# Optimization experiments

Hardware: AMD Instinct MI355X
Metric: run time of the kernel (lower is better)

## Reference

```python
import jax, jax.numpy as jnp
import numpy as np

B, H, W, C = 32, 56, 56, 192
WS, SS, NH = 7, 3, 6  # window, shift, heads
N = WS * WS
HIDDEN = int(C * 4.0)
TABLE = (2 * WS - 1) * (2 * WS - 1)  # 169
EPS = 1e-5

# Relative position index, faithful to the source (meshgrid default 'xy',
# and the source multiplies BOTH coord channels by (2*ws-1), so indices can
# exceed the table size; gather uses clip like jnp.take's jit behavior).
_coords = np.stack(np.meshgrid(np.arange(WS), np.arange(WS))).reshape(2, -1)
_rel = (_coords[:, :, None] - _coords[:, None, :]).transpose(1, 2, 0)
_rel = (_rel + WS - 1) * (2 * WS - 1)
REL_IDX = jnp.asarray(_rel.sum(-1))  # [N, N]

# Shift attention mask (static), labels regions then marks cross-region pairs.
_m = np.zeros((H, W))
_cnt = 0
for hs in [slice(0, -WS), slice(-WS, -SS), slice(-SS, None)]:
    for ws_ in [slice(0, -WS), slice(-WS, -SS), slice(-SS, None)]:
        _m[hs, ws_] = _cnt
        _cnt += 1
_mw = _m.reshape(H // WS, WS, W // WS, WS).transpose(0, 2, 1, 3).reshape(-1, N)
ATTN_MASK = jnp.asarray((_mw[:, None, :] != _mw[:, :, None]).astype(np.float32))  # [nW, N, N]
NW = ATTN_MASK.shape[0]


def layer_norm(x, g, b):
    mu = jnp.mean(x, axis=-1, keepdims=True)
    xc = x - mu
    var = jnp.mean(xc * xc, axis=-1, keepdims=True)
    return xc * jax.lax.rsqrt(var + EPS) * g + b


def window_partition(x):  # [B,H,W,C] -> [B*nW, N, C]
    x = x.reshape(B, H // WS, WS, W // WS, WS, C).transpose(0, 1, 3, 2, 4, 5)
    return x.reshape(-1, N, C)


def window_reverse(w):  # [B*nW, N, C] -> [B,H,W,C]
    x = w.reshape(B, H // WS, W // WS, WS, WS, C).transpose(0, 1, 3, 2, 4, 5)
    return x.reshape(B, H, W, C)


def setup_inputs() -> dict:
    key = jax.random.key(0)
    ks = jax.random.split(key, 16)
    s = lambda fan_in: 1.0 / np.sqrt(fan_in)
    return {
        "x": jax.random.normal(ks[0], (B, H * W, C), jnp.float32),
        "norm1_g": jnp.ones((C,), jnp.float32),
        "norm1_b": jnp.zeros((C,), jnp.float32),
        "qkv_w": jax.random.normal(ks[1], (C, 3 * C), jnp.float32) * s(C),
        "qkv_b": jnp.zeros((3 * C,), jnp.float32),
        "rel_table": jax.random.normal(ks[2], (TABLE, NH), jnp.float32) * 0.02,
        "proj_w": jax.random.normal(ks[3], (C, C), jnp.float32) * s(C),
        "proj_b": jnp.zeros((C,), jnp.float32),
        "norm2_g": jnp.ones((C,), jnp.float32),
        "norm2_b": jnp.zeros((C,), jnp.float32),
        "fc1_w": jax.random.normal(ks[4], (C, HIDDEN), jnp.float32) * s(C),
        "fc1_b": jnp.zeros((HIDDEN,), jnp.float32),
        "fc2_w": jax.random.normal(ks[5], (HIDDEN, C), jnp.float32) * s(HIDDEN),
        "fc2_b": jnp.zeros((C,), jnp.float32),
    }


def reference(x, norm1_g, norm1_b, qkv_w, qkv_b, rel_table, proj_w, proj_b,
              norm2_g, norm2_b, fc1_w, fc1_b, fc2_w, fc2_b):
    shortcut = x
    h = layer_norm(x, norm1_g, norm1_b).reshape(B, H, W, C)
    # cyclic shift
    h = jnp.roll(h, shift=(-SS, -SS), axis=(1, 2))
    xw = window_partition(h)  # [B*nW, N, C]

    # window attention
    qkv = xw @ qkv_w + qkv_b  # [B*nW, N, 3C]
    q, k, v = jnp.split(qkv, 3, axis=-1)
    hd = C // NH
    q = q.reshape(-1, N, NH, hd).transpose(0, 2, 1, 3) * (hd ** -0.5)
    k = k.reshape(-1, N, NH, hd).transpose(0, 2, 1, 3)
    v = v.reshape(-1, N, NH, hd).transpose(0, 2, 1, 3)
    attn = jnp.einsum("whnd,whmd->whnm", q, k)  # [B*nW, NH, N, N]
    bias = jnp.take(rel_table, REL_IDX, axis=0, mode="clip")  # [N,N,NH]
    attn = attn + bias.transpose(2, 0, 1)[None]
    attn = attn.reshape(B, NW, NH, N, N) + ATTN_MASK[None, :, None] * -100.0
    attn = jax.nn.softmax(attn.reshape(-1, NH, N, N), axis=-1)
    o = jnp.einsum("whnm,whmd->whnd", attn, v)
    o = o.transpose(0, 2, 1, 3).reshape(-1, N, C)
    o = o @ proj_w + proj_b

    h = window_reverse(o)
    h = jnp.roll(h, shift=(SS, SS), axis=(1, 2)).reshape(B, H * W, C)
    x = shortcut + h
    # MLP
    m = layer_norm(x, norm2_g, norm2_b)
    m = jax.nn.gelu(m @ fc1_w + fc1_b, approximate=False) @ fc2_w + fc2_b
    return x + m
```

## Files before the change

kernel.cpp:

```cpp
#include <hip/hip_runtime.h>
#include <hip/hip_bf16.h>


using f32x4  = __attribute__((ext_vector_type(4))) float;
using short8 = __attribute__((ext_vector_type(8))) short;
typedef unsigned short ushort_t;

__device__ __forceinline__ ushort_t f2bf(float f) {
    __hip_bfloat16 h = __float2bfloat16(f);
    return __builtin_bit_cast(ushort_t, h);
}
__device__ __forceinline__ f32x4 mfma16(short8 a, short8 b, f32x4 c) {
    return __builtin_amdgcn_mfma_f32_16x16x32_bf16(a, b, c, 0, 0, 0);
}
__device__ __forceinline__ float fast_gelu(float h) {
    float hh = h * h;
    float p  = __builtin_fmaf(hh, 0.044715f, 1.0f);
    float z  = h * (-1.5957691216057308f);
    float em = __expf(p * z);
    return h * __builtin_amdgcn_rcpf(1.0f + em);
}

#define CC 192

#define OFF_QKVT   0
#define OFF_PROJT  221184
#define OFF_FC1T   294912
#define OFF_FC2T   589824
#define OFF_BIAS   884736
#define OFF_MASK   942592
#define OFF_BMT    1557504
#define OFF_QG     7848960
#define OFF_KG     46384128
#define OFF_VG     84919296
#define WS_NEED    123454464
#define PREP_SMALL 610438
#define PREP_BIG   2183302

__global__ void prep_kernel(const float* __restrict__ qkv_w, const float* __restrict__ proj_w,
                            const float* __restrict__ fc1_w, const float* __restrict__ fc2_w,
                            const float* __restrict__ rel_table,
                            ushort_t* __restrict__ qkvT, ushort_t* __restrict__ projT,
                            ushort_t* __restrict__ fc1T, ushort_t* __restrict__ fc2T,
                            float* __restrict__ biasT, float* __restrict__ maskT,
                            float* __restrict__ bmT, int full) {
    int idx = blockIdx.x * 256 + threadIdx.x;
    if (idx < 110592) { int n = idx / 192, k = idx % 192; qkvT[idx] = f2bf(qkv_w[k * 576 + n]); return; }
    idx -= 110592;
    if (idx < 36864) { int n = idx / 192, k = idx % 192; projT[idx] = f2bf(proj_w[k * 192 + n]); return; }
    idx -= 36864;
    if (idx < 147456) { int n = idx / 192, k = idx % 192; fc1T[idx] = f2bf(fc1_w[k * 768 + n]); return; }
    idx -= 147456;
    if (idx < 147456) { int n = idx / 768, k = idx % 768; fc2T[idx] = f2bf(fc2_w[k * 192 + n]); return; }
    idx -= 147456;
    if (idx < 14406) {
        int h = idx / 2401; int rest = idx % 2401; int a = rest / 49, b = rest % 49;
        int d = 13 * ((a % 7) - (b % 7) + (a / 7) - (b / 7) + 12);
        if (d > 168) d = 168;
        biasT[idx] = rel_table[d * 6 + h];
        return;
    }
    idx -= 14406;
    if (idx < 153664) {
        int w = idx / 2401; int rest = idx % 2401; int a = rest / 49, b = rest % 49;
        int wy = w / 8, wx = w % 8;
        int ya = wy * 7 + a / 7, xa = wx * 7 + a % 7;
        int yb = wy * 7 + b / 7, xb = wx * 7 + b % 7;
        int lya = ya < 49 ? 0 : (ya < 53 ? 1 : 2);
        int lxa = xa < 49 ? 0 : (xa < 53 ? 1 : 2);
        int lyb = yb < 49 ? 0 : (yb < 53 ? 1 : 2);
        int lxb = xb < 49 ? 0 : (xb < 53 ? 1 : 2);
        maskT[idx] = ((lya * 3 + lxa) != (lyb * 3 + lxb)) ? -100.0f : 0.0f;
        return;
    }
    idx -= 153664;
    if (full && idx < 1572864) {
        int wi = idx / 24576; int r2 = idx % 24576;
        int h = r2 / 4096; int r3 = r2 % 4096;
        int col = r3 / 64, row = r3 % 64;
        float v = -1e30f;
        if (row < 49 && col < 49) {
            int d = 13 * ((row % 7) - (col % 7) + (row / 7) - (col / 7) + 12);
            if (d > 168) d = 168;
            float bias = rel_table[d * 6 + h];
            int wy = wi / 8, wx = wi % 8;
            int ya = wy * 7 + row / 7, xa = wx * 7 + row % 7;
            int yb = wy * 7 + col / 7, xb = wx * 7 + col % 7;
            int lya = ya < 49 ? 0 : (ya < 53 ? 1 : 2);
            int lxa = xa < 49 ? 0 : (xa < 53 ? 1 : 2);
            int lyb = yb < 49 ? 0 : (yb < 53 ? 1 : 2);
            int lxb = xb < 49 ? 0 : (xb < 53 ? 1 : 2);
            float mask = ((lya * 3 + lxa) != (lyb * 3 + lxb)) ? -100.0f : 0.0f;
            v = bias + mask;
        }
        bmT[idx] = v;
        return;
    }
}

__global__ __launch_bounds__(256, 3) void lnqkv_kernel(
    const float* __restrict__ x, const float* __restrict__ n1g, const float* __restrict__ n1b,
    const ushort_t* __restrict__ qkvT, const float* __restrict__ qkv_b,
    ushort_t* __restrict__ qg, ushort_t* __restrict__ kg, ushort_t* __restrict__ vg) {
    __shared__ ushort_t xln [64 * 200];
    __shared__ ushort_t qkvs[64 * 200];
    const int tid = threadIdx.x;
    const int wave = tid >> 6, lane = tid & 63;
    const int ln16 = lane & 15, sub = lane >> 4;
    const int t0 = blockIdx.x * 64;
    const f32x4 zero4 = {0.f, 0.f, 0.f, 0.f};

    {
        float g0 = n1g[lane], g1 = n1g[lane + 64], g2 = n1g[lane + 128];
        float bb0 = n1b[lane], bb1 = n1b[lane + 64], bb2 = n1b[lane + 128];
        for (int rb = 0; rb < 4; ++rb) {
            int row0 = wave * 16 + rb * 4;
            float v0[4], v1[4], v2[4], s[4], q[4];
            #pragma unroll
            for (int j = 0; j < 4; ++j) {
                const float* xr = x + (size_t)(t0 + row0 + j) * CC;
                v0[j] = xr[lane]; v1[j] = xr[lane + 64]; v2[j] = xr[lane + 128];
            }
            #pragma unroll
            for (int j = 0; j < 4; ++j) {
                s[j] = v0[j] + v1[j] + v2[j];
                q[j] = v0[j] * v0[j] + v1[j] * v1[j] + v2[j] * v2[j];
            }
            #pragma unroll
            for (int m = 32; m; m >>= 1) {
                #pragma unroll
                for (int j = 0; j < 4; ++j) { s[j] += __shfl_xor(s[j], m); q[j] += __shfl_xor(q[j], m); }
            }
            #pragma unroll
            for (int j = 0; j < 4; ++j) {
                float mu = s[j] * (1.0f / 192.0f);
                float var = q[j] * (1.0f / 192.0f) - mu * mu;
                float rs = rsqrtf(var + 1e-5f);
                int row = row0 + j;
                xln[row * 200 + lane]       = f2bf((v0[j] - mu) * rs * g0 + bb0);
                xln[row * 200 + lane + 64]  = f2bf((v1[j] - mu) * rs * g1 + bb1);
                xln[row * 200 + lane + 128] = f2bf((v2[j] - mu) * rs * g2 + bb2);
            }
        }
    }
    __syncthreads();

    ushort_t* dsts[3] = {qg, kg, vg};
    for (int v = 0; v < 3; ++v) {
        f32x4 acc[4][3];
        #pragma unroll
        for (int m = 0; m < 4; ++m)
            #pragma unroll
            for (int n = 0; n < 3; ++n) acc[m][n] = zero4;
        for (int kk = 0; kk < 6; ++kk) {
            short8 a[4];
            #pragma unroll
            for (int m = 0; m < 4; ++m)
                a[m] = *(const short8*)(xln + (m * 16 + ln16) * 200 + kk * 32 + 8 * sub);
            #pragma unroll
            for (int n = 0; n < 3; ++n) {
                short8 b = *(const short8*)(qkvT + (size_t)(v * 192 + (wave * 3 + n) * 16 + ln16) * 192 + kk * 32 + 8 * sub);
                #pragma unroll
                for (int m = 0; m < 4; ++m) acc[m][n] = mfma16(a[m], b, acc[m][n]);
            }
        }
        #pragma unroll
        for (int n = 0; n < 3; ++n) {
            int col = (wave * 3 + n) * 16 + ln16;
            float bv = qkv_b[v * 192 + col];
            #pragma unroll
            for (int m = 0; m < 4; ++m)
                #pragma unroll
                for (int r = 0; r < 4; ++r) {
                    int row = m * 16 + 4 * sub + r;
                    float val = acc[m][n][r] + bv;
                    if (v == 0) val *= 0.17677669529663689f;
                    qkvs[row * 200 + col] = f2bf(val);
                }
        }
        __syncthreads();
        ushort_t* dst = dsts[v];
        for (int i = tid; i < 1536; i += 256) {
            int row = i / 24, c = i % 24;
            short8 vv = *(const short8*)(qkvs + row * 200 + c * 8);
            *(short8*)(dst + (size_t)(t0 + row) * 192 + c * 8) = vv;
        }
        __syncthreads();
    }
}

__global__ __launch_bounds__(256, 3) void attnmlp_kernel(
    const float* __restrict__ x, const float* __restrict__ proj_b,
    const ushort_t* __restrict__ qg, const ushort_t* __restrict__ kg,
    const ushort_t* __restrict__ vg, const ushort_t* __restrict__ projT,
    const float* __restrict__ bmT,
    const float* __restrict__ n2g, const float* __restrict__ n2b,
    const float* __restrict__ fc1_b, const float* __restrict__ fc2_b,
    const ushort_t* __restrict__ fc1T, const ushort_t* __restrict__ fc2T,
    float* __restrict__ out) {
    __shared__ __align__(16) char smem[51200];
    ushort_t* vt   = (ushort_t*)smem;
    ushort_t* PO   = (ushort_t*)(smem + 27648);
    ushort_t* aln  = (ushort_t*)smem;
    ushort_t* hidc = (ushort_t*)(smem + 25600);
    float*    fout = (float*)smem;

    const int tid = threadIdx.x;
    const int wave = tid >> 6, lane = tid & 63;
    const int ln16 = lane & 15, sub = lane >> 4;
    const int win = blockIdx.x;
    const int b = win >> 6, wi = win & 63;
    const int wy = wi >> 3, wx = wi & 7;
    const f32x4 zero4 = {0.f, 0.f, 0.f, 0.f};

    size_t tokA;
    {
        int j = wave * 16 + ln16; if (j > 48) j = 48;
        int y  = wy * 7 + j / 7 + 3; if (y >= 56) y -= 56;
        int xx = wx * 7 + j % 7 + 3; if (xx >= 56) xx -= 56;
        tokA = (size_t)(b * 3136 + y * 56 + xx);
    }
    size_t tokB[4];
    #pragma unroll
    for (int n = 0; n < 4; ++n) {
        int j = n * 16 + ln16; if (j > 48) j = 48;
        int y  = wy * 7 + j / 7 + 3; if (y >= 56) y -= 56;
        int xx = wx * 7 + j % 7 + 3; if (xx >= 56) xx -= 56;
        tokB[n] = (size_t)(b * 3136 + y * 56 + xx);
    }
    const float* bmw = bmT + (size_t)wi * 24576 + (size_t)(wave * 16 + 4 * sub);

    short8 qf = *(const short8*)(qg + tokA * 192 + 8 * sub);
    short8 kf[4];
    f32x4  bv[4];
    #pragma unroll
    for (int n = 0; n < 4; ++n) {
        kf[n] = *(const short8*)(kg + tokB[n] * 192 + 8 * sub);
        bv[n] = *(const f32x4*)(bmw + (n * 16 + ln16) * 64);
    }

    {
        int j = tid & 63;
        int jj = j < 49 ? j : 48;
        int y  = wy * 7 + jj / 7 + 3; if (y >= 56) y -= 56;
        int xx = wx * 7 + jj % 7 + 3; if (xx >= 56) xx -= 56;
        size_t tokV = (size_t)(b * 3136 + y * 56 + xx);
        const bool valid = j < 49;
        #pragma unroll
        for (int pass = 0; pass < 6; ++pass) {
            int c8 = pass * 32 + (tid >> 6) * 8;
            if (valid) {
                short8 vv = *(const short8*)(vg + tokV * 192 + c8);
                #pragma unroll
                for (int q = 0; q < 8; ++q) vt[(c8 + q) * 72 + j] = ((ushort_t*)&vv)[q];
            } else {
                #pragma unroll
                for (int q = 0; q < 8; ++q) vt[(c8 + q) * 72 + j] = 0;
            }
        }
    }

    f32x4 accP[12];
    #pragma unroll
    for (int n = 0; n < 12; ++n) accP[n] = zero4;
    ushort_t* Pw = PO + wave * (16 * 72);
    __syncthreads();

    #pragma unroll
    for (int h = 0; h < 6; ++h) {
        f32x4 s4[4];
        #pragma unroll
        for (int n = 0; n < 4; ++n) s4[n] = mfma16(qf, kf[n], zero4);
        short8 qn; short8 kn[4]; f32x4 bn[4];
        if (h < 5) {
            qn = *(const short8*)(qg + tokA * 192 + (h + 1) * 32 + 8 * sub);
            #pragma unroll
            for (int n = 0; n < 4; ++n) {
                kn[n] = *(const short8*)(kg + tokB[n] * 192 + (h + 1) * 32 + 8 * sub);
                bn[n] = *(const f32x4*)(bmw + (h + 1) * 4096 + (n * 16 + ln16) * 64);
            }
        }
        #pragma unroll
        for (int n = 0; n < 4; ++n)
            #pragma unroll
            for (int r = 0; r < 4; ++r) s4[n][r] += bv[n][r];
        #pragma unroll
        for (int r = 0; r < 4; ++r) {
            float mx = fmaxf(fmaxf(s4[0][r], s4[1][r]), fmaxf(s4[2][r], s4[3][r]));
            mx = fmaxf(mx, __shfl_xor(mx, 1, 16));
            mx = fmaxf(mx, __shfl_xor(mx, 2, 16));
            mx = fmaxf(mx, __shfl_xor(mx, 4, 16));
            mx = fmaxf(mx, __shfl_xor(mx, 8, 16));
            float e0 = __expf(s4[0][r] - mx), e1 = __expf(s4[1][r] - mx);
            float e2 = __expf(s4[2][r] - mx), e3 = __expf(s4[3][r] - mx);
            float sm = e0 + e1 + e2 + e3;
            sm += __shfl_xor(sm, 1, 16);
            sm += __shfl_xor(sm, 2, 16);
            sm += __shfl_xor(sm, 4, 16);
            sm += __shfl_xor(sm, 8, 16);
            float inv = 1.0f / sm;
            int rl = 4 * sub + r;
            Pw[rl * 72 +      ln16] = f2bf(e0 * inv);
            Pw[rl * 72 + 16 + ln16] = f2bf(e1 * inv);
            Pw[rl * 72 + 32 + ln16] = f2bf(e2 * inv);
            Pw[rl * 72 + 48 + ln16] = f2bf(e3 * inv);
        }
        short8 ap0 = *(const short8*)(Pw + ln16 * 72 + 8 * sub);
        short8 ap1 = *(const short8*)(Pw + ln16 * 72 + 32 + 8 * sub);
        f32x4 o2[2]; o2[0] = zero4; o2[1] = zero4;
        #pragma unroll
        for (int n2 = 0; n2 < 2; ++n2) {
            short8 bv0 = *(const short8*)(vt + (h * 32 + n2 * 16 + ln16) * 72 + 8 * sub);
            short8 bv1 = *(const short8*)(vt + (h * 32 + n2 * 16 + ln16) * 72 + 32 + 8 * sub);
            o2[n2] = mfma16(ap0, bv0, o2[n2]);
            o2[n2] = mfma16(ap1, bv1, o2[n2]);
        }
        #pragma unroll
        for (int n2 = 0; n2 < 2; ++n2)
            #pragma unroll
            for (int r = 0; r < 4; ++r)
                Pw[(4 * sub + r) * 72 + n2 * 16 + ln16] = f2bf(o2[n2][r]);
        {
            short8 ao = *(const short8*)(Pw + ln16 * 72 + 8 * sub);
            #pragma unroll
            for (int n = 0; n < 12; ++n) {
                short8 bp = *(const short8*)(projT + (size_t)(n * 16 + ln16) * 192 + h * 32 + 8 * sub);
                accP[n] = mfma16(ao, bp, accP[n]);
            }
        }
        if (h < 5) {
            qf = qn;
            #pragma unroll
            for (int n = 0; n < 4; ++n) { kf[n] = kn[n]; bv[n] = bn[n]; }
        }
    }

    __syncthreads();
    for (int i = tid; i < 2352; i += 256) {
        int row = i / 48, c4 = (i % 48) * 4;
        int y  = wy * 7 + row / 7 + 3; if (y >= 56) y -= 56;
        int xx = wx * 7 + row % 7 + 3; if (xx >= 56) xx -= 56;
        const float* xp = x + (size_t)(b * 3136 + y * 56 + xx) * CC + c4;
        *(f32x4*)(fout + row * 196 + c4) = *(const f32x4*)xp;
    }
    __syncthreads();
    #pragma unroll
    for (int n = 0; n < 12; ++n) {
        int col = n * 16 + ln16;
        float pb = proj_b[col];
        #pragma unroll
        for (int r = 0; r < 4; ++r) {
            int row = wave * 16 + 4 * sub + r;
            float v = accP[n][r] + pb;
            if (row < 49) {
                v += fout[row * 196 + col];
                fout[row * 196 + col] = v;
            }
            accP[n][r] = v;
        }
    }

    float mu4[4], rs4[4];
    {
        float s[4], qs[4];
        #pragma unroll
        for (int r = 0; r < 4; ++r) { s[r] = 0.f; qs[r] = 0.f; }
        #pragma unroll
        for (int n = 0; n < 12; ++n)
            #pragma unroll
            for (int r = 0; r < 4; ++r) {
                float v = accP[n][r];
                s[r] += v; qs[r] += v * v;
            }
        #pragma unroll
        for (int m = 1; m < 16; m <<= 1) {
            #pragma unroll
            for (int r = 0; r < 4; ++r) {
                s[r]  += __shfl_xor(s[r],  m, 16);
                qs[r] += __shfl_xor(qs[r], m, 16);
            }
        }
        #pragma unroll
        for (int r = 0; r < 4; ++r) {
            float mu = s[r] * (1.0f / 192.0f);
            float var = qs[r] * (1.0f / 192.0f) - mu * mu;
            mu4[r] = mu;
            rs4[r] = rsqrtf(var + 1e-5f);
        }
    }
    __syncthreads();
    for (int i = tid; i < 2352; i += 256) {
        int row = i / 48, c4 = (i % 48) * 4;
        int y  = wy * 7 + row / 7 + 3; if (y >= 56) y -= 56;
        int xx = wx * 7 + row % 7 + 3; if (xx >= 56) xx -= 56;
        float* op = out + (size_t)(b * 3136 + y * 56 + xx) * CC + c4;
        *(f32x4*)op = *(const f32x4*)(fout + row * 196 + c4);
    }
    __threadfence_block();
    __syncthreads();

    short8 b1p[3];
    #pragma unroll
    for (int n = 0; n < 3; ++n)
        b1p[n] = *(const short8*)(fc1T + (size_t)(wave * 48 + n * 16 + ln16) * 192 + 8 * sub);

    #pragma unroll
    for (int n = 0; n < 12; ++n) {
        int col = n * 16 + ln16;
        float g = n2g[col], bb = n2b[col];
        #pragma unroll
        for (int r = 0; r < 4; ++r) {
            int row = wave * 16 + 4 * sub + r;
            aln[row * 200 + col] = f2bf((accP[n][r] - mu4[r]) * rs4[r] * g + bb);
        }
    }
    __syncthreads();

    f32x4 accO[4][3];
    #pragma unroll
    for (int m = 0; m < 4; ++m)
        #pragma unroll
        for (int n = 0; n < 3; ++n) accO[m][n] = zero4;

    for (int c = 0; c < 4; ++c) {
        f32x4 acc1[4][3];
        #pragma unroll
        for (int m = 0; m < 4; ++m)
            #pragma unroll
            for (int n = 0; n < 3; ++n) acc1[m][n] = zero4;
        #pragma unroll
        for (int kk = 0; kk < 6; ++kk) {
            short8 a[4];
            #pragma unroll
            for (int m = 0; m < 4; ++m)
                a[m] = *(const short8*)(aln + (m * 16 + ln16) * 200 + kk * 32 + 8 * sub);
            short8 bb[3];
            if (kk == 0) {
                bb[0] = b1p[0]; bb[1] = b1p[1]; bb[2] = b1p[2];
            } else {
                #pragma unroll
                for (int n = 0; n < 3; ++n)
                    bb[n] = *(const short8*)(fc1T + (size_t)(c * 192 + wave * 48 + n * 16 + ln16) * 192 + kk * 32 + 8 * sub);
            }
            __builtin_amdgcn_s_setprio(1);
            #pragma unroll
            for (int n = 0; n < 3; ++n)
                #pragma unroll
                for (int m = 0; m < 4; ++m) acc1[m][n] = mfma16(a[m], bb[n], acc1[m][n]);
            __builtin_amdgcn_s_setprio(0);
        }
        short8 b2p[3];
        #pragma unroll
        for (int n = 0; n < 3; ++n)
            b2p[n] = *(const short8*)(fc2T + (size_t)(wave * 48 + n * 16 + ln16) * 768 + c * 192 + 8 * sub);
        if (c < 3) {
            #pragma unroll
            for (int n = 0; n < 3; ++n)
                b1p[n] = *(const short8*)(fc1T + (size_t)((c + 1) * 192 + wave * 48 + n * 16 + ln16) * 192 + 8 * sub);
        }
        #pragma unroll
        for (int n = 0; n < 3; ++n) {
            int cl = wave * 48 + n * 16 + ln16;
            float fb = fc1_b[c * 192 + cl];
            #pragma unroll
            for (int m = 0; m < 4; ++m)
                #pragma unroll
                for (int r = 0; r < 4; ++r) {
                    float hv = acc1[m][n][r] + fb;
                    hidc[(m * 16 + 4 * sub + r) * 200 + cl] = f2bf(fast_gelu(hv));
                }
        }
        __syncthreads();
        #pragma unroll
        for (int kk = 0; kk < 6; ++kk) {
            short8 a[4];
            #pragma unroll
            for (int m = 0; m < 4; ++m)
                a[m] = *(const short8*)(hidc + (m * 16 + ln16) * 200 + kk * 32 + 8 * sub);
            short8 bb[3];
            if (kk == 0) {
                bb[0] = b2p[0]; bb[1] = b2p[1]; bb[2] = b2p[2];
            } else {
                #pragma unroll
                for (int n = 0; n < 3; ++n)
                    bb[n] = *(const short8*)(fc2T + (size_t)(wave * 48 + n * 16 + ln16) * 768 + c * 192 + kk * 32 + 8 * sub);
            }
            __builtin_amdgcn_s_setprio(1);
            #pragma unroll
            for (int n = 0; n < 3; ++n)
                #pragma unroll
                for (int m = 0; m < 4; ++m) accO[m][n] = mfma16(a[m], bb[n], accO[m][n]);
            __builtin_amdgcn_s_setprio(0);
        }
        __syncthreads();
    }

    #pragma unroll
    for (int n = 0; n < 3; ++n) {
        int col = wave * 48 + n * 16 + ln16;
        float fb = fc2_b[col];
        #pragma unroll
        for (int m = 0; m < 4; ++m)
            #pragma unroll
            for (int r = 0; r < 4; ++r)
                fout[(m * 16 + 4 * sub + r) * 196 + col] = accO[m][n][r] + fb;
    }
    __syncthreads();
    for (int i = tid; i < 2352; i += 256) {
        int row = i / 48, c4 = (i % 48) * 4;
        int y  = wy * 7 + row / 7 + 3; if (y >= 56) y -= 56;
        int xx = wx * 7 + row % 7 + 3; if (xx >= 56) xx -= 56;
        float* op = out + (size_t)(b * 3136 + y * 56 + xx) * CC + c4;
        f32x4 sv = *(const f32x4*)(fout + row * 196 + c4);
        f32x4 ov = *(const f32x4*)op;
        #pragma unroll
        for (int q = 0; q < 4; ++q) ov[q] += sv[q];
        *(f32x4*)op = ov;
    }
}

__global__ __launch_bounds__(256, 3) void attn_kernel(
    const float* __restrict__ x, const float* __restrict__ n1g, const float* __restrict__ n1b,
    const float* __restrict__ qkv_b, const float* __restrict__ proj_b,
    const ushort_t* __restrict__ qkvT, const ushort_t* __restrict__ projT,
    const float* __restrict__ biasT, const float* __restrict__ maskT,
    float* __restrict__ out) {
    __shared__ ushort_t xln[64 * 200];
    __shared__ ushort_t qo [64 * 40];
    __shared__ ushort_t kl [64 * 40];
    __shared__ ushort_t vt [32 * 72];
    __shared__ ushort_t Pl [64 * 72];
    const int tid = threadIdx.x;
    const int wave = tid >> 6, lane = tid & 63;
    const int ln16 = lane & 15, sub = lane >> 4;
    const int w = blockIdx.x;
    const int batch = w >> 6, wi = w & 63;
    const int wy = wi >> 3, wx = wi & 7;
    const f32x4 zero4 = {0.f, 0.f, 0.f, 0.f};

    for (int rr = 0; rr < 16; ++rr) {
        int row = wave * 16 + rr;
        if (row < 49) {
            int ty = row / 7, tx = row % 7;
            int y  = wy * 7 + ty + 3; if (y >= 56) y -= 56;
            int xx = wx * 7 + tx + 3; if (xx >= 56) xx -= 56;
            const float* xr = x + (size_t)(batch * 3136 + y * 56 + xx) * CC;
            float v0 = xr[lane], v1 = xr[lane + 64], v2 = xr[lane + 128];
            float s = v0 + v1 + v2;
            #pragma unroll
            for (int m = 32; m; m >>= 1) s += __shfl_xor(s, m);
            float mu = s * (1.0f / 192.0f);
            float d0 = v0 - mu, d1 = v1 - mu, d2 = v2 - mu;
            float q = d0 * d0 + d1 * d1 + d2 * d2;
            #pragma unroll
            for (int m = 32; m; m >>= 1) q += __shfl_xor(q, m);
            float rs = rsqrtf(q * (1.0f / 192.0f) + 1e-5f);
            xln[row * 200 + lane]       = f2bf(d0 * rs * n1g[lane]       + n1b[lane]);
            xln[row * 200 + lane + 64]  = f2bf(d1 * rs * n1g[lane + 64]  + n1b[lane + 64]);
            xln[row * 200 + lane + 128] = f2bf(d2 * rs * n1g[lane + 128] + n1b[lane + 128]);
        } else {
            xln[row * 200 + lane] = 0; xln[row * 200 + lane + 64] = 0; xln[row * 200 + lane + 128] = 0;
        }
    }

    f32x4 accP[12];
    #pragma unroll
    for (int n = 0; n < 12; ++n) accP[n] = zero4;
    const float scale = 0.17677669529663689f;
    const float* mptr = maskT + wi * 2401;

    for (int h = 0; h < 6; ++h) {
        f32x4 acc6[6];
        #pragma unroll
        for (int n = 0; n < 6; ++n) acc6[n] = zero4;
        const int cb0 = h * 32;
        for (int kk = 0; kk < 6; ++kk) {
            short8 a = *(const short8*)(xln + (wave * 16 + ln16) * 200 + kk * 32 + 8 * sub);
            #pragma unroll
            for (int n = 0; n < 6; ++n) {
                int colbase = (n >> 1) * 192 + cb0 + (n & 1) * 16;
                short8 b = *(const short8*)(qkvT + (size_t)(colbase + ln16) * 192 + kk * 32 + 8 * sub);
                acc6[n] = mfma16(a, b, acc6[n]);
            }
        }
        #pragma unroll
        for (int n = 0; n < 6; ++n) {
            int colbase = (n >> 1) * 192 + cb0 + (n & 1) * 16;
            float bv = qkv_b[colbase + ln16];
            int dim = (n & 1) * 16 + ln16;
            #pragma unroll
            for (int r = 0; r < 4; ++r) {
                int row = wave * 16 + 4 * sub + r;
                ushort_t hv = f2bf(acc6[n][r] + bv);
                if (n < 2)      qo[row * 40 + dim] = hv;
                else if (n < 4) kl[row * 40 + dim] = hv;
                else            vt[dim * 72 + row] = hv;
            }
        }
        __syncthreads();

        f32x4 s4[4];
        {
            short8 aq = *(const short8*)(qo + (wave * 16 + ln16) * 40 + 8 * sub);
            #pragma unroll
            for (int n = 0; n < 4; ++n) {
                short8 bk = *(const short8*)(kl + (n * 16 + ln16) * 40 + 8 * sub);
                s4[n] = mfma16(aq, bk, zero4);
            }
        }
        const float* bptr = biasT + h * 2401;
        #pragma unroll
        for (int n = 0; n < 4; ++n) {
            int col = n * 16 + ln16;
            #pragma unroll
            for (int r = 0; r < 4; ++r) {
                int row = wave * 16 + 4 * sub + r;
                s4[n][r] = (row < 49 && col < 49)
                    ? s4[n][r] * scale + bptr[row * 49 + col] + mptr[row * 49 + col]
                    : -1e30f;
            }
        }
        #pragma unroll
        for (int r = 0; r < 4; ++r) {
            float mx = fmaxf(fmaxf(s4[0][r], s4[1][r]), fmaxf(s4[2][r], s4[3][r]));
            mx = fmaxf(mx, __shfl_xor(mx, 1, 16));
            mx = fmaxf(mx, __shfl_xor(mx, 2, 16));
            mx = fmaxf(mx, __shfl_xor(mx, 4, 16));
            mx = fmaxf(mx, __shfl_xor(mx, 8, 16));
            float e0 = __expf(s4[0][r] - mx), e1 = __expf(s4[1][r] - mx);
            float e2 = __expf(s4[2][r] - mx), e3 = __expf(s4[3][r] - mx);
            float sm = e0 + e1 + e2 + e3;
            sm += __shfl_xor(sm, 1, 16);
            sm += __shfl_xor(sm, 2, 16);
            sm += __shfl_xor(sm, 4, 16);
            sm += __shfl_xor(sm, 8, 16);
            float inv = 1.0f / sm;
            int row = wave * 16 + 4 * sub + r;
            Pl[row * 72 +      ln16] = f2bf(e0 * inv);
            Pl[row * 72 + 16 + ln16] = f2bf(e1 * inv);
            Pl[row * 72 + 32 + ln16] = f2bf(e2 * inv);
            Pl[row * 72 + 48 + ln16] = f2bf(e3 * inv);
        }
        f32x4 o2[2]; o2[0] = zero4; o2[1] = zero4;
        #pragma unroll
        for (int ks = 0; ks < 2; ++ks) {
            short8 ap = *(const short8*)(Pl + (wave * 16 + ln16) * 72 + ks * 32 + 8 * sub);
            #pragma unroll
            for (int n2 = 0; n2 < 2; ++n2) {
                short8 bv = *(const short8*)(vt + (n2 * 16 + ln16) * 72 + ks * 32 + 8 * sub);
                o2[n2] = mfma16(ap, bv, o2[n2]);
            }
        }
        #pragma unroll
        for (int n2 = 0; n2 < 2; ++n2)
            #pragma unroll
            for (int r = 0; r < 4; ++r) {
                int row = wave * 16 + 4 * sub + r;
                qo[row * 40 + n2 * 16 + ln16] = f2bf(o2[n2][r]);
            }
        {
            short8 ao = *(const short8*)(qo + (wave * 16 + ln16) * 40 + 8 * sub);
            #pragma unroll
            for (int n = 0; n < 12; ++n) {
                short8 bp = *(const short8*)(projT + (size_t)(n * 16 + ln16) * 192 + h * 32 + 8 * sub);
                accP[n] = mfma16(ao, bp, accP[n]);
            }
        }
        __syncthreads();
    }

    #pragma unroll
    for (int n = 0; n < 12; ++n) {
        int col = n * 16 + ln16;
        float pb = proj_b[col];
        #pragma unroll
        for (int r = 0; r < 4; ++r) {
            int row = wave * 16 + 4 * sub + r;
            if (row < 49) {
                int ty = row / 7, tx = row % 7;
                int y  = wy * 7 + ty + 3; if (y >= 56) y -= 56;
                int xx = wx * 7 + tx + 3; if (xx >= 56) xx -= 56;
                size_t g = (size_t)(batch * 3136 + y * 56 + xx) * CC;
                out[g + col] = accP[n][r] + pb + x[g + col];
            }
        }
    }
}

__global__ __launch_bounds__(256, 3) void mlp5_kernel(
    float* __restrict__ out, const float* __restrict__ n2g, const float* __restrict__ n2b,
    const float* __restrict__ fc1_b, const float* __restrict__ fc2_b,
    const ushort_t* __restrict__ fc1T, const ushort_t* __restrict__ fc2T) {
    __shared__ ushort_t smem[2][64 * 200];
    ushort_t* aln  = smem[0];
    ushort_t* hidc = smem[1];
    float* fout = (float*)&smem[0][0];
    const int tid = threadIdx.x;
    const int wave = tid >> 6, lane = tid & 63;
    const int ln16 = lane & 15, sub = lane >> 4;
    const size_t t0 = (size_t)blockIdx.x * 64;
    const f32x4 zero4 = {0.f, 0.f, 0.f, 0.f};

    short8 b1p[3];
    #pragma unroll
    for (int n = 0; n < 3; ++n)
        b1p[n] = *(const short8*)(fc1T + (size_t)(wave * 48 + n * 16 + ln16) * 192 + 8 * sub);

    {
        float g0 = n2g[lane], g1 = n2g[lane + 64], g2 = n2g[lane + 128];
        float bb0 = n2b[lane], bb1 = n2b[lane + 64], bb2 = n2b[lane + 128];
        for (int rb = 0; rb < 4; ++rb) {
            int row0 = wave * 16 + rb * 4;
            float v0[4], v1[4], v2[4], s[4], q[4];
            #pragma unroll
            for (int j = 0; j < 4; ++j) {
                const float* xr = out + (t0 + row0 + j) * CC;
                v0[j] = xr[lane]; v1[j] = xr[lane + 64]; v2[j] = xr[lane + 128];
            }
            #pragma unroll
            for (int j = 0; j < 4; ++j) {
                s[j] = v0[j] + v1[j] + v2[j];
                q[j] = v0[j] * v0[j] + v1[j] * v1[j] + v2[j] * v2[j];
            }
            #pragma unroll
            for (int m = 32; m; m >>= 1) {
                #pragma unroll
                for (int j = 0; j < 4; ++j) { s[j] += __shfl_xor(s[j], m); q[j] += __shfl_xor(q[j], m); }
            }
            #pragma unroll
            for (int j = 0; j < 4; ++j) {
                float mu = s[j] * (1.0f / 192.0f);
                float var = q[j] * (1.0f / 192.0f) - mu * mu;
                float rs = rsqrtf(var + 1e-5f);
                int row = row0 + j;
                aln[row * 200 + lane]       = f2bf((v0[j] - mu) * rs * g0 + bb0);
                aln[row * 200 + lane + 64]  = f2bf((v1[j] - mu) * rs * g1 + bb1);
                aln[row * 200 + lane + 128] = f2bf((v2[j] - mu) * rs * g2 + bb2);
            }
        }
    }
    __syncthreads();

    f32x4 accO[4][3];
    #pragma unroll
    for (int m = 0; m < 4; ++m)
        #pragma unroll
        for (int n = 0; n < 3; ++n) accO[m][n] = zero4;

    for (int c = 0; c < 4; ++c) {
        f32x4 acc1[4][3];
        #pragma unroll
        for (int m = 0; m < 4; ++m)
            #pragma unroll
            for (int n = 0; n < 3; ++n) acc1[m][n] = zero4;
        #pragma unroll
        for (int kk = 0; kk < 6; ++kk) {
            short8 a[4];
            #pragma unroll
            for (int m = 0; m < 4; ++m)
                a[m] = *(const short8*)(aln + (m * 16 + ln16) * 200 + kk * 32 + 8 * sub);
            short8 bb[3];
            if (kk == 0) {
                bb[0] = b1p[0]; bb[1] = b1p[1]; bb[2] = b1p[2];
            } else {
                #pragma unroll
                for (int n = 0; n < 3; ++n)
                    bb[n] = *(const short8*)(fc1T + (size_t)(c * 192 + wave * 48 + n * 16 + ln16) * 192 + kk * 32 + 8 * sub);
            }
            __builtin_amdgcn_s_setprio(1);
            #pragma unroll
            for (int n = 0; n < 3; ++n)
                #pragma unroll
                for (int m = 0; m < 4; ++m) acc1[m][n] = mfma16(a[m], bb[n], acc1[m][n]);
            __builtin_amdgcn_s_setprio(0);
        }
        short8 b2p[3];
        #pragma unroll
        for (int n = 0; n < 3; ++n)
            b2p[n] = *(const short8*)(fc2T + (size_t)(wave * 48 + n * 16 + ln16) * 768 + c * 192 + 8 * sub);
        if (c < 3) {
            #pragma unroll
            for (int n = 0; n < 3; ++n)
                b1p[n] = *(const short8*)(fc1T + (size_t)((c + 1) * 192 + wave * 48 + n * 16 + ln16) * 192 + 8 * sub);
        }
        #pragma unroll
        for (int n = 0; n < 3; ++n) {
            int cl = wave * 48 + n * 16 + ln16;
            float fb = fc1_b[c * 192 + cl];
            #pragma unroll
            for (int m = 0; m < 4; ++m)
                #pragma unroll
                for (int r = 0; r < 4; ++r) {
                    float hv = acc1[m][n][r] + fb;
                    hidc[(m * 16 + 4 * sub + r) * 200 + cl] = f2bf(fast_gelu(hv));
                }
        }
        __syncthreads();
        #pragma unroll
        for (int kk = 0; kk < 6; ++kk) {
            short8 a[4];
            #pragma unroll
            for (int m = 0; m < 4; ++m)
                a[m] = *(const short8*)(hidc + (m * 16 + ln16) * 200 + kk * 32 + 8 * sub);
            short8 bb[3];
            if (kk == 0) {
                bb[0] = b2p[0]; bb[1] = b2p[1]; bb[2] = b2p[2];
            } else {
                #pragma unroll
                for (int n = 0; n < 3; ++n)
                    bb[n] = *(const short8*)(fc2T + (size_t)(wave * 48 + n * 16 + ln16) * 768 + c * 192 + kk * 32 + 8 * sub);
            }
            __builtin_amdgcn_s_setprio(1);
            #pragma unroll
            for (int n = 0; n < 3; ++n)
                #pragma unroll
                for (int m = 0; m < 4; ++m) accO[m][n] = mfma16(a[m], bb[n], accO[m][n]);
            __builtin_amdgcn_s_setprio(0);
        }
        __syncthreads();
    }

    #pragma unroll
    for (int n = 0; n < 3; ++n) {
        int col = wave * 48 + n * 16 + ln16;
        float fb = fc2_b[col];
        #pragma unroll
        for (int m = 0; m < 4; ++m)
            #pragma unroll
            for (int r = 0; r < 4; ++r)
                fout[(m * 16 + 4 * sub + r) * 196 + col] = accO[m][n][r] + fb;
    }
    __syncthreads();
    for (int i = tid; i < 3072; i += 256) {
        int row = i / 48, c4 = (i % 48) * 4;
        f32x4 sv = *(const f32x4*)(fout + row * 196 + c4);
        float* op = out + (t0 + row) * CC + c4;
        f32x4 ov = *(const f32x4*)op;
        #pragma unroll
        for (int q = 0; q < 4; ++q) ov[q] += sv[q];
        *(f32x4*)op = ov;
    }
}

extern "C" void kernel_launch(void* const* d_in, const int* in_sizes, int n_in,
                              void* d_out, int out_size, void* d_ws, size_t ws_size,
                              hipStream_t stream) {
    const float* x      = (const float*)d_in[0];
    const float* n1g    = (const float*)d_in[1];
    const float* n1b    = (const float*)d_in[2];
    const float* qkv_w  = (const float*)d_in[3];
    const float* qkv_b  = (const float*)d_in[4];
    const float* rel_t  = (const float*)d_in[5];
    const float* proj_w = (const float*)d_in[6];
    const float* proj_b = (const float*)d_in[7];
    const float* n2g    = (const float*)d_in[8];
    const float* n2b    = (const float*)d_in[9];
    const float* fc1_w  = (const float*)d_in[10];
    const float* fc1_b  = (const float*)d_in[11];
    const float* fc2_w  = (const float*)d_in[12];
    const float* fc2_b  = (const float*)d_in[13];
    float* out = (float*)d_out;

    char* ws = (char*)d_ws;
    ushort_t* qkvT  = (ushort_t*)(ws + OFF_QKVT);
    ushort_t* projT = (ushort_t*)(ws + OFF_PROJT);
    ushort_t* fc1T  = (ushort_t*)(ws + OFF_FC1T);
    ushort_t* fc2T  = (ushort_t*)(ws + OFF_FC2T);
    float* biasT    = (float*)(ws + OFF_BIAS);
    float* maskT    = (float*)(ws + OFF_MASK);
    float* bmT      = (float*)(ws + OFF_BMT);
    ushort_t* qg    = (ushort_t*)(ws + OFF_QG);
    ushort_t* kg    = (ushort_t*)(ws + OFF_KG);
    ushort_t* vg    = (ushort_t*)(ws + OFF_VG);

    const int big = ws_size >= (size_t)WS_NEED;
    const int prep_total = big ? PREP_BIG : PREP_SMALL;
    prep_kernel<<<(prep_total + 255) / 256, 256, 0, stream>>>(
        qkv_w, proj_w, fc1_w, fc2_w, rel_t, qkvT, projT, fc1T, fc2T, biasT, maskT, bmT, big);

    if (big) {
        lnqkv_kernel<<<1568, 256, 0, stream>>>(x, n1g, n1b, qkvT, qkv_b, qg, kg, vg);
        attnmlp_kernel<<<2048, 256, 0, stream>>>(x, proj_b, qg, kg, vg, projT, bmT,
                                                 n2g, n2b, fc1_b, fc2_b, fc1T, fc2T, out);
    } else {
        attn_kernel<<<2048, 256, 0, stream>>>(x, n1g, n1b, qkv_b, proj_b,
                                              qkvT, projT, biasT, maskT, out);
        mlp5_kernel<<<1568, 256, 0, stream>>>(out, n2g, n2b, fc1_b, fc2_b, fc1T, fc2T);
    }
}
```

Measured before the change: 405.6 us.

## Chunk MLP hidden dimension into 64-wide slices to cut LDS and raise occupancy

```diff
diff --git a/kernel.cpp b/kernel.cpp
--- a/kernel.cpp
+++ b/kernel.cpp
@@ -189,7 +189,7 @@
     }
 }
 
-__global__ __launch_bounds__(256, 3) void attnmlp_kernel(
+__global__ __launch_bounds__(256, 4) void attnmlp_kernel(
     const float* __restrict__ x, const float* __restrict__ proj_b,
     const ushort_t* __restrict__ qg, const ushort_t* __restrict__ kg,
     const ushort_t* __restrict__ vg, const ushort_t* __restrict__ projT,
@@ -198,7 +198,7 @@
     const float* __restrict__ fc1_b, const float* __restrict__ fc2_b,
     const ushort_t* __restrict__ fc1T, const ushort_t* __restrict__ fc2T,
     float* __restrict__ out) {
-    __shared__ __align__(16) char smem[51200];
+    __shared__ __align__(16) char smem[38416];
     ushort_t* vt   = (ushort_t*)smem;
     ushort_t* PO   = (ushort_t*)(smem + 27648);
     ushort_t* aln  = (ushort_t*)smem;
@@ -399,10 +399,7 @@
     __threadfence_block();
     __syncthreads();
 
-    short8 b1p[3];
-    #pragma unroll
-    for (int n = 0; n < 3; ++n)
-        b1p[n] = *(const short8*)(fc1T + (size_t)(wave * 48 + n * 16 + ln16) * 192 + 8 * sub);
+    short8 b1p = *(const short8*)(fc1T + (size_t)(wave * 16 + ln16) * 192 + 8 * sub);
 
     #pragma unroll
     for (int n = 0; n < 12; ++n) {
@@ -422,68 +419,54 @@
         #pragma unroll
         for (int n = 0; n < 3; ++n) accO[m][n] = zero4;
 
-    for (int c = 0; c < 4; ++c) {
-        f32x4 acc1[4][3];
-        #pragma unroll
-        for (int m = 0; m < 4; ++m)
-            #pragma unroll
-            for (int n = 0; n < 3; ++n) acc1[m][n] = zero4;
+    for (int c = 0; c < 12; ++c) {
+        f32x4 acc1[4];
+        #pragma unroll
+        for (int m = 0; m < 4; ++m) acc1[m] = zero4;
         #pragma unroll
         for (int kk = 0; kk < 6; ++kk) {
             short8 a[4];
             #pragma unroll
             for (int m = 0; m < 4; ++m)
                 a[m] = *(const short8*)(aln + (m * 16 + ln16) * 200 + kk * 32 + 8 * sub);
-            short8 bb[3];
-            if (kk == 0) {
-                bb[0] = b1p[0]; bb[1] = b1p[1]; bb[2] = b1p[2];
-            } else {
-                #pragma unroll
-                for (int n = 0; n < 3; ++n)
-                    bb[n] = *(const short8*)(fc1T + (size_t)(c * 192 + wave * 48 + n * 16 + ln16) * 192 + kk * 32 + 8 * sub);
-            }
+            short8 bb = (kk == 0) ? b1p
+                : *(const short8*)(fc1T + (size_t)(c * 64 + wave * 16 + ln16) * 192 + kk * 32 + 8 * sub);
             __builtin_amdgcn_s_setprio(1);
             #pragma unroll
-            for (int n = 0; n < 3; ++n)
-                #pragma unroll
-                for (int m = 0; m < 4; ++m) acc1[m][n] = mfma16(a[m], bb[n], acc1[m][n]);
+            for (int m = 0; m < 4; ++m) acc1[m] = mfma16(a[m], bb, acc1[m]);
             __builtin_amdgcn_s_setprio(0);
         }
         short8 b2p[3];
         #pragma unroll
         for (int n = 0; n < 3; ++n)
-            b2p[n] = *(const short8*)(fc2T + (size_t)(wave * 48 + n * 16 + ln16) * 768 + c * 192 + 8 * sub);
-        if (c < 3) {
-            #pragma unroll
-            for (int n = 0; n < 3; ++n)
-                b1p[n] = *(const short8*)(fc1T + (size_t)((c + 1) * 192 + wave * 48 + n * 16 + ln16) * 192 + 8 * sub);
-        }
-        #pragma unroll
-        for (int n = 0; n < 3; ++n) {
-            int cl = wave * 48 + n * 16 + ln16;
-            float fb = fc1_b[c * 192 + cl];
+            b2p[n] = *(const short8*)(fc2T + (size_t)(wave * 48 + n * 16 + ln16) * 768 + c * 64 + 8 * sub);
+        if (c < 11)
+            b1p = *(const short8*)(fc1T + (size_t)((c + 1) * 64 + wave * 16 + ln16) * 192 + 8 * sub);
+        {
+            int cl = wave * 16 + ln16;
+            float fb = fc1_b[c * 64 + cl];
             #pragma unroll
             for (int m = 0; m < 4; ++m)
                 #pragma unroll
                 for (int r = 0; r < 4; ++r) {
-                    float hv = acc1[m][n][r] + fb;
-                    hidc[(m * 16 + 4 * sub + r) * 200 + cl] = f2bf(fast_gelu(hv));
+                    float hv = acc1[m][r] + fb;
+                    hidc[(m * 16 + 4 * sub + r) * 72 + cl] = f2bf(fast_gelu(hv));
                 }
         }
         __syncthreads();
         #pragma unroll
-        for (int kk = 0; kk < 6; ++kk) {
+        for (int kk = 0; kk < 2; ++kk) {
             short8 a[4];
             #pragma unroll
             for (int m = 0; m < 4; ++m)
-                a[m] = *(const short8*)(hidc + (m * 16 + ln16) * 200 + kk * 32 + 8 * sub);
+                a[m] = *(const short8*)(hidc + (m * 16 + ln16) * 72 + kk * 32 + 8 * sub);
             short8 bb[3];
             if (kk == 0) {
                 bb[0] = b2p[0]; bb[1] = b2p[1]; bb[2] = b2p[2];
             } else {
                 #pragma unroll
                 for (int n = 0; n < 3; ++n)
-                    bb[n] = *(const short8*)(fc2T + (size_t)(wave * 48 + n * 16 + ln16) * 768 + c * 192 + kk * 32 + 8 * sub);
+                    bb[n] = *(const short8*)(fc2T + (size_t)(wave * 48 + n * 16 + ln16) * 768 + c * 64 + kk * 32 + 8 * sub);
             }
             __builtin_amdgcn_s_setprio(1);
             #pragma unroll
@@ -502,8 +485,10 @@
         #pragma unroll
         for (int m = 0; m < 4; ++m)
             #pragma unroll
-            for (int r = 0; r < 4; ++r)
-                fout[(m * 16 + 4 * sub + r) * 196 + col] = accO[m][n][r] + fb;
+            for (int r = 0; r < 4; ++r) {
+                int row = m * 16 + 4 * sub + r;
+                if (row < 49) fout[row * 196 + col] = accO[m][n][r] + fb;
+            }
     }
     __syncthreads();
     for (int i = tid; i < 2352; i += 256) {
```

Measured after the change: 398.4 us. No clear change (-1.8%).
